# Kernel tuning notes

Hardware: AMD Instinct MI355X
Metric: run time of the kernel (lower is better)

Reference implementation:

```python
import jax, jax.numpy as jnp
import numpy as np
from jax.ops import segment_sum

N_NODES = 100000
N_EDGES = 1600000
N_GRAPHS = 64
IN_DIM = 128
HID = 128
N_CLASSES = 10


def setup_inputs() -> dict:
    key = jax.random.key(0)
    ks = jax.random.split(key, 8)
    h = jax.random.normal(ks[0], (N_NODES, IN_DIM), dtype=jnp.float32)
    src = jax.random.randint(ks[1], (N_EDGES,), 0, N_NODES, dtype=jnp.int64)
    dst = jax.random.randint(ks[2], (N_EDGES,), 0, N_NODES, dtype=jnp.int64)
    graph_ids = jnp.sort(jax.random.randint(ks[3], (N_NODES,), 0, N_GRAPHS, dtype=jnp.int64))
    # Glorot-ish scaled weights
    W1 = jax.random.normal(ks[4], (IN_DIM, HID), dtype=jnp.float32) / np.sqrt(IN_DIM)
    b1 = jnp.zeros((HID,), dtype=jnp.float32)
    W2 = jax.random.normal(ks[5], (HID, HID), dtype=jnp.float32) / np.sqrt(HID)
    b2 = jnp.zeros((HID,), dtype=jnp.float32)
    Wc = jax.random.normal(ks[6], (HID, N_CLASSES), dtype=jnp.float32) / np.sqrt(HID)
    bc = jnp.zeros((N_CLASSES,), dtype=jnp.float32)
    return {"h": h, "src": src, "dst": dst, "graph_ids": graph_ids,
            "W1": W1, "b1": b1, "W2": W2, "b2": b2, "Wc": Wc, "bc": bc}


def _graph_conv(h, src, dst, W, b, n_nodes):
    # DGL GraphConv, norm='both': D_out^{-1/2} scaling of src feats,
    # sum aggregation over edges, D_in^{-1/2} scaling of dst, then XW + b.
    ones = jnp.ones((src.shape[0],), dtype=h.dtype)
    deg_out = jnp.clip(segment_sum(ones, src, num_segments=n_nodes), 1.0)
    deg_in = jnp.clip(segment_sum(ones, dst, num_segments=n_nodes), 1.0)
    hn = h * jax.lax.rsqrt(deg_out)[:, None]          # [N, d]
    agg = segment_sum(hn[src], dst, num_segments=n_nodes)  # SpMM: [N, d]
    agg = agg * jax.lax.rsqrt(deg_in)[:, None]
    return agg @ W + b


def reference(h, src, dst, graph_ids, W1, b1, W2, b2, Wc, bc):
    n = h.shape[0]
    x = jax.nn.relu(_graph_conv(h, src, dst, W1, b1, n))
    x = jax.nn.relu(_graph_conv(x, src, dst, W2, b2, n))
    # mean_nodes readout per graph
    counts = jnp.clip(segment_sum(jnp.ones((n,), x.dtype), graph_ids, num_segments=N_GRAPHS), 1.0)
    hg = segment_sum(x, graph_ids, num_segments=N_GRAPHS) / counts[:, None]  # [G, d]
    return hg @ Wc + bc  # [G, n_classes]
```

## Files before the change

### kernel.cpp

```cpp
#include <hip/hip_runtime.h>

#define DIM 128
#define NG 64
#define NCLS 10
#define CAP 64
#define WSZ 256
#define NWMAX 512
#define CAPB 8192
#define EPB 8192
#define HL 4

typedef __attribute__((ext_vector_type(8))) short s8v;
typedef __attribute__((ext_vector_type(4))) float f4v;

__device__ inline unsigned short f2bf(float f) {
    unsigned int u = __float_as_uint(f);
    unsigned int r = (u + 0x7fffu + ((u >> 16) & 1u)) >> 16;
    return (unsigned short)r;
}
__device__ inline unsigned int pack2bf(float a, float b) {
    return ((unsigned int)f2bf(b) << 16) | (unsigned int)f2bf(a);
}

__global__ void init_cursors(int* curD, int* curS, int nw) {
    int t = blockIdx.x * 256 + threadIdx.x;
    if (t < nw) {
        curD[t] = t * CAPB;
        curS[t] = t * CAPB;
    }
}

__global__ __launch_bounds__(256) void bucket_kernel(const int* __restrict__ src,
                                                     const int* __restrict__ dst,
                                                     int* curD, int* curS,
                                                     int* __restrict__ bucketD,
                                                     unsigned char* __restrict__ bucketS,
                                                     int e, int nw) {
    __shared__ int histD[NWMAX];
    __shared__ int histS[NWMAX];
    int t = threadIdx.x;
    for (int i = t; i < nw; i += 256) { histD[i] = 0; histS[i] = 0; }
    __syncthreads();
    int lo = blockIdx.x * EPB;
    int hi = min(e, lo + EPB);
    for (int i = lo + t * 4; i < hi; i += 1024) {
        int4 d4 = *(const int4*)&dst[i];
        int4 s4 = *(const int4*)&src[i];
        atomicAdd(&histD[d4.x >> 8], 1); atomicAdd(&histS[s4.x >> 8], 1);
        atomicAdd(&histD[d4.y >> 8], 1); atomicAdd(&histS[s4.y >> 8], 1);
        atomicAdd(&histD[d4.z >> 8], 1); atomicAdd(&histS[s4.z >> 8], 1);
        atomicAdd(&histD[d4.w >> 8], 1); atomicAdd(&histS[s4.w >> 8], 1);
    }
    __syncthreads();
    for (int i = t; i < nw; i += 256) {
        int hd = histD[i], hs = histS[i];
        histD[i] = hd ? atomicAdd(&curD[i], hd) : 0;
        histS[i] = hs ? atomicAdd(&curS[i], hs) : 0;
    }
    __syncthreads();
    for (int i = lo + t * 4; i < hi; i += 1024) {
        int4 d4 = *(const int4*)&dst[i];
        int4 s4 = *(const int4*)&src[i];
#pragma unroll
        for (int j = 0; j < 4; ++j) {
            int d = (&d4.x)[j], s = (&s4.x)[j];
            int sd = atomicAdd(&histD[d >> 8], 1);
            bucketD[sd] = (s << 8) | (d & 255);
            int ss = atomicAdd(&histS[s >> 8], 1);
            bucketS[ss] = (unsigned char)(s & 255);
        }
    }
}

__global__ __launch_bounds__(256) void window_kernel(const int* __restrict__ curD,
                                                     const int* __restrict__ curS,
                                                     const int* __restrict__ bucketD,
                                                     const unsigned char* __restrict__ bucketS,
                                                     int* __restrict__ cnt_in,
                                                     float* __restrict__ rs_in,
                                                     float* __restrict__ rs_out,
                                                     int* __restrict__ colx_pad, int n) {
    __shared__ int cin[WSZ];
    __shared__ int cout[WSZ];
    int w = blockIdx.x, t = threadIdx.x;
    cin[t] = 0;
    cout[t] = 0;
    __syncthreads();
    int base = w * CAPB;
    int nE = min(curD[w] - base, CAPB);
    for (int i = t; i < nE; i += 256) {
        int v = bucketD[base + i];
        int d8 = v & 255;
        int slot = atomicAdd(&cin[d8], 1);
        if (slot < CAP) colx_pad[(((w << 8) + d8) << 6) + slot] = v >> 8;
    }
    int nS = min(curS[w] - base, CAPB);
    for (int i = t; i < nS; i += 256) atomicAdd(&cout[bucketS[base + i]], 1);
    __syncthreads();
    int node = (w << 8) + t;
    if (node < n) {
        int c = cin[t];
        cnt_in[node] = c;
        rs_in[node] = rsqrtf(fmaxf((float)c, 1.0f));
        rs_out[node] = rsqrtf(fmaxf((float)cout[t], 1.0f));
    }
}

__global__ void cast_scale_kernel(const float* __restrict__ x, const float* __restrict__ rs_out,
                                  unsigned int* __restrict__ y, int total2) {
    int i = blockIdx.x * 256 + threadIdx.x;
    if (i < total2) {
        float s = rs_out[i >> 6];
        float2 v = ((const float2*)x)[i];
        y[i] = pack2bf(v.x * s, v.y * s);
    }
}

__global__ void cast_wt2_kernel(const float* __restrict__ W1, const float* __restrict__ W2,
                                unsigned short* __restrict__ Wt1,
                                unsigned short* __restrict__ Wt2) {
    int t = blockIdx.x * 256 + threadIdx.x;
    int which = t >> 14;
    int i = t & 16383;
    int c = i >> 7, k = i & 127;
    const float* W = which ? W2 : W1;
    unsigned short* Wt = which ? Wt2 : Wt1;
    Wt[i] = f2bf(W[k * 128 + c]);
}

__global__ __launch_bounds__(256) void spmm_bf16(const unsigned int* __restrict__ xb,
                                                 const int* __restrict__ cnt_in,
                                                 const int* __restrict__ colx_pad,
                                                 const float* __restrict__ rs_in,
                                                 unsigned int* __restrict__ yb, int n) {
    int node = (blockIdx.x * 256 + threadIdx.x) >> 6;
    int lane = threadIdx.x & 63;
    if (node >= n) return;
    int cnt = min(cnt_in[node], CAP);
    int myc = colx_pad[(node << 6) + ((lane < cnt) ? lane : 0)];
    float ax = 0.0f, ay = 0.0f;
    int j = 0;
    for (; j + 16 <= cnt; j += 16) {
        unsigned int v[16];
#pragma unroll
        for (int q = 0; q < 16; ++q) {
            int c = __shfl(myc, j + q);
            v[q] = xb[(size_t)c * 64 + lane];
        }
#pragma unroll
        for (int q = 0; q < 16; ++q) {
            ax += __uint_as_float(v[q] << 16);
            ay += __uint_as_float(v[q] & 0xffff0000u);
        }
    }
    for (; j + 8 <= cnt; j += 8) {
        unsigned int v[8];
#pragma unroll
        for (int q = 0; q < 8; ++q) {
            int c = __shfl(myc, j + q);
            v[q] = xb[(size_t)c * 64 + lane];
        }
#pragma unroll
        for (int q = 0; q < 8; ++q) {
            ax += __uint_as_float(v[q] << 16);
            ay += __uint_as_float(v[q] & 0xffff0000u);
        }
    }
    for (; j < cnt; ++j) {
        int c = __shfl(myc, j);
        unsigned int v = xb[(size_t)c * 64 + lane];
        ax += __uint_as_float(v << 16);
        ay += __uint_as_float(v & 0xffff0000u);
    }
    float w = rs_in[node];
    yb[(size_t)node * 64 + lane] = pack2bf(ax * w, ay * w);
}

__global__ __launch_bounds__(256) void mm_mfma(const unsigned char* __restrict__ A,
                                               const unsigned char* __restrict__ Wt,
                                               const float* __restrict__ bias,
                                               const float* __restrict__ rs_out,
                                               unsigned short* __restrict__ out, int n) {
    int wave = threadIdx.x >> 6, lane = threadIdx.x & 63;
    int m = lane & 15, q = lane >> 4;
    int r0 = (int)blockIdx.x * 64 + wave * 16;
    int arow = min(r0 + m, n - 1);
    f4v acc[8];
#pragma unroll
    for (int c = 0; c < 8; ++c) acc[c] = (f4v){0.f, 0.f, 0.f, 0.f};
#pragma unroll
    for (int k0 = 0; k0 < 4; ++k0) {
        s8v a = *(const s8v*)(A + (size_t)arow * 256 + k0 * 64 + q * 16);
#pragma unroll
        for (int c = 0; c < 8; ++c) {
            s8v b = *(const s8v*)(Wt + (size_t)(c * 16 + m) * 256 + k0 * 64 + q * 16);
            acc[c] = __builtin_amdgcn_mfma_f32_16x16x32_bf16(a, b, acc[c], 0, 0, 0);
        }
    }
#pragma unroll
    for (int c = 0; c < 8; ++c) {
        float bv = bias[c * 16 + m];
#pragma unroll
        for (int r = 0; r < 4; ++r) {
            int row = r0 + q * 4 + r;
            if (row < n) {
                float val = fmaxf(acc[c][r] + bv, 0.0f);
                out[(size_t)row * 128 + c * 16 + m] = f2bf(val * rs_out[row]);
            }
        }
    }
}

__global__ __launch_bounds__(256) void mm_mfma_readout(const unsigned char* __restrict__ A,
                                                       const unsigned char* __restrict__ Wt,
                                                       const float* __restrict__ bias,
                                                       const int* __restrict__ gid,
                                                       float* __restrict__ hg, int n) {
    __shared__ float hgloc[HL][DIM];
    int wave = threadIdx.x >> 6, lane = threadIdx.x & 63;
    int m = lane & 15, q = lane >> 4;
    int r0 = (int)blockIdx.x * 64 + wave * 16;
    int b0 = (int)blockIdx.x * 64;
    int gid0 = gid[min(b0, n - 1)];
    for (int i = threadIdx.x; i < HL * DIM; i += 256) ((float*)hgloc)[i] = 0.0f;
    __syncthreads();
    int arow = min(r0 + m, n - 1);
    f4v acc[8];
#pragma unroll
    for (int c = 0; c < 8; ++c) acc[c] = (f4v){0.f, 0.f, 0.f, 0.f};
#pragma unroll
    for (int k0 = 0; k0 < 4; ++k0) {
        s8v a = *(const s8v*)(A + (size_t)arow * 256 + k0 * 64 + q * 16);
#pragma unroll
        for (int c = 0; c < 8; ++c) {
            s8v b = *(const s8v*)(Wt + (size_t)(c * 16 + m) * 256 + k0 * 64 + q * 16);
            acc[c] = __builtin_amdgcn_mfma_f32_16x16x32_bf16(a, b, acc[c], 0, 0, 0);
        }
    }
    int gfirst = gid[min(r0, n - 1)];
    int glast = gid[min(r0 + 15, n - 1)];
    bool uni = (gfirst == glast) && (r0 + 15 < n);
    if (uni) {
        int gl = gfirst - gid0;
#pragma unroll
        for (int c = 0; c < 8; ++c) {
            float bv = bias[c * 16 + m];
            float s = fmaxf(acc[c][0] + bv, 0.0f) + fmaxf(acc[c][1] + bv, 0.0f) +
                      fmaxf(acc[c][2] + bv, 0.0f) + fmaxf(acc[c][3] + bv, 0.0f);
            s += __shfl_xor(s, 16);
            s += __shfl_xor(s, 32);
            if (q == 0) {
                if (gl < HL)
                    atomicAdd(&hgloc[gl][c * 16 + m], s);
                else
                    atomicAdd(&hg[(size_t)gfirst * DIM + c * 16 + m], s);
            }
        }
    } else {
#pragma unroll
        for (int r = 0; r < 4; ++r) {
            int row = r0 + q * 4 + r;
            if (row < n) {
                int g = gid[row];
                int gl = g - gid0;
#pragma unroll
                for (int c = 0; c < 8; ++c) {
                    float val = fmaxf(acc[c][r] + bias[c * 16 + m], 0.0f);
                    if (gl < HL)
                        atomicAdd(&hgloc[gl][c * 16 + m], val);
                    else
                        atomicAdd(&hg[(size_t)g * DIM + c * 16 + m], val);
                }
            }
        }
    }
    __syncthreads();
    for (int i = threadIdx.x; i < HL * DIM; i += 256) {
        float v = ((float*)hgloc)[i];
        int g = gid0 + (i >> 7);
        if (v != 0.0f && g < NG) atomicAdd(&hg[(size_t)g * DIM + (i & 127)], v);
    }
}

__global__ void classify_kernel(const float* __restrict__ hg, const int* __restrict__ gid,
                                const float* __restrict__ Wc, const float* __restrict__ bc,
                                float* __restrict__ out, int n) {
    __shared__ float inv[NG];
    int t = threadIdx.x;
    if (t < NG) {
        int g = t;
        int lo = 0, hi = n;
        while (lo < hi) { int mid = (lo + hi) >> 1; if (gid[mid] < g) lo = mid + 1; else hi = mid; }
        int lb = lo;
        lo = 0; hi = n;
        while (lo < hi) { int mid = (lo + hi) >> 1; if (gid[mid] <= g) lo = mid + 1; else hi = mid; }
        inv[t] = 1.0f / fmaxf((float)(lo - lb), 1.0f);
    }
    __syncthreads();
    for (int idx = t; idx < NG * NCLS; idx += 256) {
        int g = idx / NCLS, c = idx % NCLS;
        float s = 0.0f;
        for (int k = 0; k < DIM; ++k) s = fmaf(hg[g * DIM + k], Wc[k * NCLS + c], s);
        out[idx] = s * inv[g] + bc[c];
    }
}

extern "C" void kernel_launch(void* const* d_in, const int* in_sizes, int n_in,
                              void* d_out, int out_size, void* d_ws, size_t ws_size,
                              hipStream_t stream) {
    const float* h   = (const float*)d_in[0];
    const int*   src = (const int*)d_in[1];
    const int*   dst = (const int*)d_in[2];
    const int*   gid = (const int*)d_in[3];
    const float* W1  = (const float*)d_in[4];
    const float* b1  = (const float*)d_in[5];
    const float* W2  = (const float*)d_in[6];
    const float* b2  = (const float*)d_in[7];
    const float* Wc  = (const float*)d_in[8];
    const float* bc  = (const float*)d_in[9];
    float* out = (float*)d_out;

    const int n = in_sizes[0] / DIM;
    const int e = in_sizes[1];
    const int nw = (n + WSZ - 1) / WSZ;

    char* ws = (char*)d_ws;
    size_t off = 0;
    auto alloc = [&](size_t bytes) -> char* {
        char* p = ws + off;
        off = (off + bytes + 255) & ~(size_t)255;
        return p;
    };
    int*   cnt_in  = (int*)alloc((size_t)n * 4);
    float* rs_in   = (float*)alloc((size_t)n * 4);
    float* rs_out  = (float*)alloc((size_t)n * 4);
    int*   curD    = (int*)alloc((size_t)NWMAX * 4);
    int*   curS    = (int*)alloc((size_t)NWMAX * 4);
    int*   colx_pad = (int*)alloc((size_t)n * CAP * 4);
    int*   bucketD = (int*)alloc((size_t)nw * CAPB * 4);
    unsigned char* bucketS = (unsigned char*)alloc((size_t)nw * CAPB);
    float* hg      = (float*)alloc((size_t)NG * DIM * 4);
    unsigned short* Wt1 = (unsigned short*)alloc(128 * 128 * 2);
    unsigned short* Wt2 = (unsigned short*)alloc(128 * 128 * 2);
    unsigned int* hb   = (unsigned int*)alloc((size_t)n * 64 * 4);
    unsigned int* aggB = (unsigned int*)alloc((size_t)n * 64 * 4);
    unsigned int* x1b  = (unsigned int*)alloc((size_t)n * 64 * 4);

    const int SPMM_B = (n + 3) / 4;
    const int MM_B = (n + 63) / 64;
    const int C2 = n * 64;
    const int AB = (e + EPB - 1) / EPB;

    (void)hipMemsetAsync(hg, 0, (size_t)NG * DIM * 4, stream);

    init_cursors<<<(nw + 255) / 256, 256, 0, stream>>>(curD, curS, nw);
    bucket_kernel<<<AB, 256, 0, stream>>>(src, dst, curD, curS, bucketD, bucketS, e, nw);
    window_kernel<<<nw, 256, 0, stream>>>(curD, curS, bucketD, bucketS,
                                          cnt_in, rs_in, rs_out, colx_pad, n);

    cast_wt2_kernel<<<128, 256, 0, stream>>>(W1, W2, Wt1, Wt2);
    cast_scale_kernel<<<(C2 + 255) / 256, 256, 0, stream>>>(h, rs_out, hb, C2);

    spmm_bf16<<<SPMM_B, 256, 0, stream>>>(hb, cnt_in, colx_pad, rs_in, aggB, n);
    mm_mfma<<<MM_B, 256, 0, stream>>>((const unsigned char*)aggB,
                                      (const unsigned char*)Wt1, b1, rs_out, (unsigned short*)x1b, n);
    spmm_bf16<<<SPMM_B, 256, 0, stream>>>(x1b, cnt_in, colx_pad, rs_in, aggB, n);
    mm_mfma_readout<<<MM_B, 256, 0, stream>>>((const unsigned char*)aggB,
                                              (const unsigned char*)Wt2, b2, gid, hg, n);
    classify_kernel<<<1, 256, 0, stream>>>(hg, gid, Wc, bc, out, n);
}
```

Before: 386.7 us.

## Widen SpMM gathers to 16-byte rows, fuse cast into window kernel, merge prep kernels

The SpMM now has each 16-lane quarter-wave gather a whole 256-byte bf16 row with uint4 loads, handling four edges per step, then reduces the partial sums across quarters with xor shuffles. Padding the neighbour lists to a multiple of four with a zero dummy row (index n) removes the scalar tail loop. The scale-and-cast of h to bf16 moves into the window kernel, and the cursor init and weight transpose are merged into one prep kernel, cutting launches. The classifier is spread over one block per graph. The cost is extra shuffle reductions, wasted lanes on padded edges, and more work inside the window kernel.

```diff
diff --git a/kernel.cpp b/kernel.cpp
--- a/kernel.cpp
+++ b/kernel.cpp
@@ -22,11 +22,24 @@
     return ((unsigned int)f2bf(b) << 16) | (unsigned int)f2bf(a);
 }
 
-__global__ void init_cursors(int* curD, int* curS, int nw) {
+__global__ void prep_kernel(const float* __restrict__ W1, const float* __restrict__ W2,
+                            unsigned short* __restrict__ Wt1, unsigned short* __restrict__ Wt2,
+                            int* curD, int* curS, uint4* hb4, uint4* x1b4, int nw, int n) {
     int t = blockIdx.x * 256 + threadIdx.x;
     if (t < nw) {
         curD[t] = t * CAPB;
         curS[t] = t * CAPB;
+    }
+    if (t < 32768) {
+        int which = t >> 14;
+        int i = t & 16383;
+        int c = i >> 7, k = i & 127;
+        (which ? Wt2 : Wt1)[i] = f2bf((which ? W2 : W1)[k * 128 + c]);
+    }
+    if (t < 16) {
+        uint4 z = make_uint4(0, 0, 0, 0);
+        hb4[(size_t)n * 16 + t] = z;
+        x1b4[(size_t)n * 16 + t] = z;
     }
 }
 
@@ -76,12 +89,15 @@
                                                      const int* __restrict__ curS,
                                                      const int* __restrict__ bucketD,
                                                      const unsigned char* __restrict__ bucketS,
+                                                     const float* __restrict__ h,
                                                      int* __restrict__ cnt_in,
                                                      float* __restrict__ rs_in,
                                                      float* __restrict__ rs_out,
-                                                     int* __restrict__ colx_pad, int n) {
+                                                     int* __restrict__ colx_pad,
+                                                     uint4* __restrict__ hb4, int n) {
     __shared__ int cin[WSZ];
     __shared__ int cout[WSZ];
+    __shared__ float rsO_s[WSZ];
     int w = blockIdx.x, t = threadIdx.x;
     cin[t] = 0;
     cout[t] = 0;
@@ -102,78 +118,90 @@
         int c = cin[t];
         cnt_in[node] = c;
         rs_in[node] = rsqrtf(fmaxf((float)c, 1.0f));
-        rs_out[node] = rsqrtf(fmaxf((float)cout[t], 1.0f));
-    }
-}
-
-__global__ void cast_scale_kernel(const float* __restrict__ x, const float* __restrict__ rs_out,
-                                  unsigned int* __restrict__ y, int total2) {
-    int i = blockIdx.x * 256 + threadIdx.x;
-    if (i < total2) {
-        float s = rs_out[i >> 6];
-        float2 v = ((const float2*)x)[i];
-        y[i] = pack2bf(v.x * s, v.y * s);
-    }
-}
-
-__global__ void cast_wt2_kernel(const float* __restrict__ W1, const float* __restrict__ W2,
-                                unsigned short* __restrict__ Wt1,
-                                unsigned short* __restrict__ Wt2) {
-    int t = blockIdx.x * 256 + threadIdx.x;
-    int which = t >> 14;
-    int i = t & 16383;
-    int c = i >> 7, k = i & 127;
-    const float* W = which ? W2 : W1;
-    unsigned short* Wt = which ? Wt2 : Wt1;
-    Wt[i] = f2bf(W[k * 128 + c]);
-}
-
-__global__ __launch_bounds__(256) void spmm_bf16(const unsigned int* __restrict__ xb,
+        float ro = rsqrtf(fmaxf((float)cout[t], 1.0f));
+        rs_out[node] = ro;
+        rsO_s[t] = ro;
+        int cc = min(c, CAP);
+        int c4 = min((cc + 3) & ~3, CAP);
+        for (int s = cc; s < c4; ++s) colx_pad[((size_t)node << 6) + s] = n;
+    }
+    __syncthreads();
+    for (int idx = t; idx < WSZ * 16; idx += 256) {
+        int rl = idx >> 4, sub = idx & 15;
+        int nd = (w << 8) + rl;
+        if (nd < n) {
+            float s = rsO_s[rl];
+            float4 a = ((const float4*)h)[(size_t)nd * 32 + sub * 2];
+            float4 b = ((const float4*)h)[(size_t)nd * 32 + sub * 2 + 1];
+            uint4 o;
+            o.x = pack2bf(a.x * s, a.y * s);
+            o.y = pack2bf(a.z * s, a.w * s);
+            o.z = pack2bf(b.x * s, b.y * s);
+            o.w = pack2bf(b.z * s, b.w * s);
+            hb4[(size_t)nd * 16 + sub] = o;
+        }
+    }
+}
+
+__global__ __launch_bounds__(256) void spmm_bf16(const uint4* __restrict__ xb4,
                                                  const int* __restrict__ cnt_in,
                                                  const int* __restrict__ colx_pad,
                                                  const float* __restrict__ rs_in,
-                                                 unsigned int* __restrict__ yb, int n) {
+                                                 uint4* __restrict__ yb4, int n) {
     int node = (blockIdx.x * 256 + threadIdx.x) >> 6;
     int lane = threadIdx.x & 63;
     if (node >= n) return;
+    int g = lane >> 4, sub = lane & 15;
     int cnt = min(cnt_in[node], CAP);
-    int myc = colx_pad[(node << 6) + ((lane < cnt) ? lane : 0)];
-    float ax = 0.0f, ay = 0.0f;
+    int cnt4 = min((cnt + 3) & ~3, CAP);
+    int myc = colx_pad[((size_t)node << 6) + ((lane < cnt4) ? lane : 0)];
+    float acc[8] = {0.f, 0.f, 0.f, 0.f, 0.f, 0.f, 0.f, 0.f};
     int j = 0;
-    for (; j + 16 <= cnt; j += 16) {
-        unsigned int v[16];
-#pragma unroll
-        for (int q = 0; q < 16; ++q) {
-            int c = __shfl(myc, j + q);
-            v[q] = xb[(size_t)c * 64 + lane];
-        }
-#pragma unroll
-        for (int q = 0; q < 16; ++q) {
-            ax += __uint_as_float(v[q] << 16);
-            ay += __uint_as_float(v[q] & 0xffff0000u);
-        }
-    }
-    for (; j + 8 <= cnt; j += 8) {
-        unsigned int v[8];
-#pragma unroll
-        for (int q = 0; q < 8; ++q) {
-            int c = __shfl(myc, j + q);
-            v[q] = xb[(size_t)c * 64 + lane];
-        }
-#pragma unroll
-        for (int q = 0; q < 8; ++q) {
-            ax += __uint_as_float(v[q] << 16);
-            ay += __uint_as_float(v[q] & 0xffff0000u);
-        }
-    }
-    for (; j < cnt; ++j) {
-        int c = __shfl(myc, j);
-        unsigned int v = xb[(size_t)c * 64 + lane];
-        ax += __uint_as_float(v << 16);
-        ay += __uint_as_float(v & 0xffff0000u);
-    }
-    float w = rs_in[node];
-    yb[(size_t)node * 64 + lane] = pack2bf(ax * w, ay * w);
+    for (; j + 16 <= cnt4; j += 16) {
+        uint4 v[4];
+#pragma unroll
+        for (int b = 0; b < 4; ++b) {
+            int c = __shfl(myc, j + 4 * b + g);
+            v[b] = xb4[(size_t)c * 16 + sub];
+        }
+#pragma unroll
+        for (int b = 0; b < 4; ++b) {
+            acc[0] += __uint_as_float(v[b].x << 16);
+            acc[1] += __uint_as_float(v[b].x & 0xffff0000u);
+            acc[2] += __uint_as_float(v[b].y << 16);
+            acc[3] += __uint_as_float(v[b].y & 0xffff0000u);
+            acc[4] += __uint_as_float(v[b].z << 16);
+            acc[5] += __uint_as_float(v[b].z & 0xffff0000u);
+            acc[6] += __uint_as_float(v[b].w << 16);
+            acc[7] += __uint_as_float(v[b].w & 0xffff0000u);
+        }
+    }
+    for (; j < cnt4; j += 4) {
+        int c = __shfl(myc, j + g);
+        uint4 v = xb4[(size_t)c * 16 + sub];
+        acc[0] += __uint_as_float(v.x << 16);
+        acc[1] += __uint_as_float(v.x & 0xffff0000u);
+        acc[2] += __uint_as_float(v.y << 16);
+        acc[3] += __uint_as_float(v.y & 0xffff0000u);
+        acc[4] += __uint_as_float(v.z << 16);
+        acc[5] += __uint_as_float(v.z & 0xffff0000u);
+        acc[6] += __uint_as_float(v.w << 16);
+        acc[7] += __uint_as_float(v.w & 0xffff0000u);
+    }
+#pragma unroll
+    for (int i = 0; i < 8; ++i) {
+        acc[i] += __shfl_xor(acc[i], 16);
+        acc[i] += __shfl_xor(acc[i], 32);
+    }
+    if (g == 0) {
+        float w = rs_in[node];
+        uint4 o;
+        o.x = pack2bf(acc[0] * w, acc[1] * w);
+        o.y = pack2bf(acc[2] * w, acc[3] * w);
+        o.z = pack2bf(acc[4] * w, acc[5] * w);
+        o.w = pack2bf(acc[6] * w, acc[7] * w);
+        yb4[(size_t)node * 16 + sub] = o;
+    }
 }
 
 __global__ __launch_bounds__(256) void mm_mfma(const unsigned char* __restrict__ A,
@@ -285,23 +313,21 @@
 __global__ void classify_kernel(const float* __restrict__ hg, const int* __restrict__ gid,
                                 const float* __restrict__ Wc, const float* __restrict__ bc,
                                 float* __restrict__ out, int n) {
-    __shared__ float inv[NG];
-    int t = threadIdx.x;
-    if (t < NG) {
-        int g = t;
+    __shared__ float inv;
+    int g = blockIdx.x, t = threadIdx.x;
+    if (t == 0) {
         int lo = 0, hi = n;
         while (lo < hi) { int mid = (lo + hi) >> 1; if (gid[mid] < g) lo = mid + 1; else hi = mid; }
         int lb = lo;
         lo = 0; hi = n;
         while (lo < hi) { int mid = (lo + hi) >> 1; if (gid[mid] <= g) lo = mid + 1; else hi = mid; }
-        inv[t] = 1.0f / fmaxf((float)(lo - lb), 1.0f);
-    }
-    __syncthreads();
-    for (int idx = t; idx < NG * NCLS; idx += 256) {
-        int g = idx / NCLS, c = idx % NCLS;
+        inv = 1.0f / fmaxf((float)(lo - lb), 1.0f);
+    }
+    __syncthreads();
+    if (t < NCLS) {
         float s = 0.0f;
-        for (int k = 0; k < DIM; ++k) s = fmaf(hg[g * DIM + k], Wc[k * NCLS + c], s);
-        out[idx] = s * inv[g] + bc[c];
+        for (int k = 0; k < DIM; ++k) s = fmaf(hg[g * DIM + k], Wc[k * NCLS + t], s);
+        out[g * NCLS + t] = s * inv + bc[t];
     }
 }
 
@@ -342,30 +368,27 @@
     float* hg      = (float*)alloc((size_t)NG * DIM * 4);
     unsigned short* Wt1 = (unsigned short*)alloc(128 * 128 * 2);
     unsigned short* Wt2 = (unsigned short*)alloc(128 * 128 * 2);
-    unsigned int* hb   = (unsigned int*)alloc((size_t)n * 64 * 4);
-    unsigned int* aggB = (unsigned int*)alloc((size_t)n * 64 * 4);
-    unsigned int* x1b  = (unsigned int*)alloc((size_t)n * 64 * 4);
+    uint4* hb4  = (uint4*)alloc((size_t)(n + 4) * 64 * 4);
+    uint4* aggB = (uint4*)alloc((size_t)(n + 4) * 64 * 4);
+    uint4* x1b4 = (uint4*)alloc((size_t)(n + 4) * 64 * 4);
 
     const int SPMM_B = (n + 3) / 4;
     const int MM_B = (n + 63) / 64;
-    const int C2 = n * 64;
     const int AB = (e + EPB - 1) / EPB;
 
     (void)hipMemsetAsync(hg, 0, (size_t)NG * DIM * 4, stream);
 
-    init_cursors<<<(nw + 255) / 256, 256, 0, stream>>>(curD, curS, nw);
+    prep_kernel<<<128, 256, 0, stream>>>(W1, W2, Wt1, Wt2, curD, curS, hb4, x1b4, nw, n);
     bucket_kernel<<<AB, 256, 0, stream>>>(src, dst, curD, curS, bucketD, bucketS, e, nw);
-    window_kernel<<<nw, 256, 0, stream>>>(curD, curS, bucketD, bucketS,
-                                          cnt_in, rs_in, rs_out, colx_pad, n);
-
-    cast_wt2_kernel<<<128, 256, 0, stream>>>(W1, W2, Wt1, Wt2);
-    cast_scale_kernel<<<(C2 + 255) / 256, 256, 0, stream>>>(h, rs_out, hb, C2);
-
-    spmm_bf16<<<SPMM_B, 256, 0, stream>>>(hb, cnt_in, colx_pad, rs_in, aggB, n);
+    window_kernel<<<nw, 256, 0, stream>>>(curD, curS, bucketD, bucketS, h,
+                                          cnt_in, rs_in, rs_out, colx_pad, hb4, n);
+
+    spmm_bf16<<<SPMM_B, 256, 0, stream>>>(hb4, cnt_in, colx_pad, rs_in, aggB, n);
     mm_mfma<<<MM_B, 256, 0, stream>>>((const unsigned char*)aggB,
-                                      (const unsigned char*)Wt1, b1, rs_out, (unsigned short*)x1b, n);
-    spmm_bf16<<<SPMM_B, 256, 0, stream>>>(x1b, cnt_in, colx_pad, rs_in, aggB, n);
+                                      (const unsigned char*)Wt1, b1, rs_out,
+                                      (unsigned short*)x1b4, n);
+    spmm_bf16<<<SPMM_B, 256, 0, stream>>>(x1b4, cnt_in, colx_pad, rs_in, aggB, n);
     mm_mfma_readout<<<MM_B, 256, 0, stream>>>((const unsigned char*)aggB,
                                               (const unsigned char*)Wt2, b2, gid, hg, n);
-    classify_kernel<<<1, 256, 0, stream>>>(hg, gid, Wc, bc, out, n);
-}
+    classify_kernel<<<NG, 64, 0, stream>>>(hg, gid, Wc, bc, out, n);
+}
```

Result: faster. 363.1 us (-6.1%).
